# Performance work log

Measured on AMD Instinct MI355X. Metric: run time of the kernel, lower is better.

## Reference

```python
import jax, jax.numpy as jnp
import numpy as np

B, L, D, HW = 128, 512, 512, 512
NEG = -1e9


def _ff(x, weights):
    # feed-forward chain: relu(x @ W) per layer
    for w in weights:
        x = jax.nn.relu(jnp.matmul(x, w))
    return x


def _masked_softmax_flat(logits, mask):
    # softmax over the flattened last axis, masked entries excluded
    logits = jnp.where(mask > 0, logits, NEG)
    return jax.nn.softmax(logits, axis=-1)


def setup_inputs() -> dict:
    key = jax.random.key(0)
    ks = jax.random.split(key, 11)
    u = lambda k, shape: jax.random.uniform(k, shape, jnp.float32, -0.05, 0.05)
    return {
        "premise": jax.random.normal(ks[0], (B, L, D), jnp.float32),
        "hypothesis": jax.random.normal(ks[1], (B, L, D), jnp.float32),
        "premise_mask": jax.random.randint(ks[2], (B, L), 0, 2, jnp.int32),
        "hypothesis_mask": jax.random.randint(ks[3], (B, L), 0, 2, jnp.int32),
        "attend_w0": u(ks[4], (D, HW)),
        "attend_w1": u(ks[5], (HW, HW)),
        "compare_w0": u(ks[6], (2 * D, HW)),
        "compare_w1": u(ks[7], (HW, HW)),
        "aggregate_w0": u(ks[8], (2 * HW, HW)),
        "aggregate_w1": u(ks[9], (HW, HW)),
        "scorer": u(ks[10], (HW, 2)),
    }


def reference(premise, hypothesis, premise_mask, hypothesis_mask,
              attend_w0, attend_w1, compare_w0, compare_w1,
              aggregate_w0, aggregate_w1, scorer):
    pm = premise_mask.astype(premise.dtype)      # [B, P]
    hm = hypothesis_mask.astype(hypothesis.dtype)  # [B, H]
    p_emb = premise * pm[..., None]              # zero out masked words
    h_emb = hypothesis * hm[..., None]

    # Attend: project with shared F, score all pairs
    proj_p = _ff(p_emb, [attend_w0, attend_w1])  # [B, P, HW]
    proj_h = _ff(h_emb, [attend_w0, attend_w1])  # [B, H, HW]
    att = jnp.einsum('bpd,bhd->bph', proj_p, proj_h)  # [B, P, H]
    Bn, P, H = att.shape

    # Faithful to original: softmax over the *flattened* P*H axis with pairwise mask
    p2h_mask = (pm[:, :, None] * hm[:, None, :]).reshape(Bn, P * H)
    h2p_mask = (hm[:, :, None] * pm[:, None, :]).reshape(Bn, H * P)
    p2h = _masked_softmax_flat(att.reshape(Bn, P * H), p2h_mask).reshape(Bn, P, H)
    h2p = _masked_softmax_flat(jnp.swapaxes(att, 1, 2).reshape(Bn, H * P), h2p_mask).reshape(Bn, H, P)

    # Weighted sums (alignments)
    p2h_align = jnp.einsum('bph,bhd->bpd', p2h, h_emb)  # [B, P, D]
    h2p_align = jnp.einsum('bhp,bpd->bhd', h2p, p_emb)  # [B, H, D]

    # Compare with shared G
    compared_p = _ff(jnp.concatenate([p_emb, p2h_align], axis=-1), [compare_w0, compare_w1])
    compared_h = _ff(jnp.concatenate([h_emb, h2p_align], axis=-1), [compare_w0, compare_w1])

    # Aggregate with H, then score
    aggregated = jnp.concatenate([compared_p.sum(axis=1), compared_h.sum(axis=1)], axis=-1)  # [B, 2*HW]
    hidden = _ff(aggregated, [aggregate_w0, aggregate_w1])  # [B, HW]
    return jax.nn.softmax(jnp.matmul(hidden, scorer), axis=-1)  # [B, 2]
```

## Files before the change

### kernel.cpp

```cpp
#include <hip/hip_runtime.h>
#include <hip/hip_bf16.h>
#include <stdint.h>

typedef unsigned short u16;
typedef uint8_t u8;
typedef __bf16 bf16x8 __attribute__((ext_vector_type(8)));
typedef float f32x4 __attribute__((ext_vector_type(4)));

__device__ __forceinline__ u16 f2b(float f){
  uint32_t u = __float_as_uint(f);
  u = (u + 0x7fffu + ((u >> 16) & 1u)) >> 16;
  return (u16)u;
}
__device__ __forceinline__ float b2f(u16 u){
  return __uint_as_float(((uint32_t)u) << 16);
}
__device__ __forceinline__ uint32_t f2e4(float f){
  uint32_t u = __float_as_uint(f);
  uint32_t s = (u >> 24) & 0x80u;
  uint32_t a = u & 0x7fffffffu;
  if (a >= 0x43e00000u) return s | 0x7eu;
  if (a < 0x3c800000u){
    float v = __uint_as_float(a) * 512.0f + 12582912.0f;
    return s | (__float_as_uint(v) & 7u);
  }
  uint32_t t = a - (120u << 23);
  t += 0x7ffffu + ((t >> 20) & 1u);
  return s | (t >> 20);
}

typedef const void __attribute__((address_space(1))) gv_t;
typedef void __attribute__((address_space(3))) sv_t;

__device__ __forceinline__ void gload16(const void* g, void* l){
  __builtin_amdgcn_global_load_lds((gv_t*)g, (sv_t*)l, 16, 0, 0);
}

__global__ __launch_bounds__(256) void cnt_scan(const int* __restrict__ pm,
    const int* __restrict__ hm, int* __restrict__ pfx, int* __restrict__ cnts)
{
  int bs = blockIdx.x;
  const int* msk = (bs < 128) ? pm + bs*512 : hm + (bs-128)*512;
  __shared__ int sA[256], sB[256], fl[512];
  int t = threadIdx.x;
  int a = (msk[2*t] != 0), b = (msk[2*t+1] != 0);
  fl[2*t] = a; fl[2*t+1] = b;
  sA[t] = a + b;
  __syncthreads();
  int* cur = sA; int* nxt = sB;
  #pragma unroll
  for (int off = 1; off < 256; off <<= 1){
    int v = cur[t] + ((t >= off) ? cur[t-off] : 0);
    nxt[t] = v;
    __syncthreads();
    int* tmp = cur; cur = nxt; nxt = tmp;
  }
  int incl = cur[t];
  int excl = incl - fl[2*t] - fl[2*t+1];
  pfx[bs*512 + 2*t]     = excl;
  pfx[bs*512 + 2*t + 1] = excl + fl[2*t];
  if (t == 255) cnts[bs] = incl;
}

__global__ __launch_bounds__(256) void gscan_k(const int* __restrict__ cnts,
    int* __restrict__ gpfx, int* __restrict__ hloc)
{
  __shared__ int sA[256], sB[256];
  int t = threadIdx.x;
  int v0 = cnts[t];
  sA[t] = v0;
  __syncthreads();
  int* cur = sA; int* nxt = sB;
  #pragma unroll
  for (int off = 1; off < 256; off <<= 1){
    int v = cur[t] + ((t >= off) ? cur[t-off] : 0);
    nxt[t] = v;
    __syncthreads();
    int* tmp = cur; cur = nxt; nxt = tmp;
  }
  int incl = cur[t];
  gpfx[t] = incl - v0;
  if (t == 255) gpfx[256] = incl;
  __syncthreads();
  if (t >= 128) hloc[t - 128] = (incl - v0) - cur[127];
}

__global__ __launch_bounds__(256) void compact_copy(
    const float* __restrict__ prem, const float* __restrict__ hyp,
    const int* __restrict__ pm, const int* __restrict__ hm,
    const int* __restrict__ pfx, const int* __restrict__ gpfx,
    u8* __restrict__ embC8, int* __restrict__ rowMap)
{
  int blk = blockIdx.x;
  int bs = blk >> 2, qtr = blk & 3;
  const float* src = (bs < 128) ? prem + (long)bs*262144 : hyp + (long)(bs-128)*262144;
  const int*  msk = (bs < 128) ? pm + bs*512 : hm + (bs-128)*512;
  const int*  pf  = pfx + bs*512;
  long gbase = gpfx[bs];
  int t = threadIdx.x;
  for (int idx = t; idx < 128*32; idx += 256){
    int r = qtr*128 + (idx >> 5);
    if (msk[r] == 0) continue;
    int c = (idx & 31) * 16;
    int dr = pf[r];
    long g = gbase + dr;
    if ((idx & 31) == 0) rowMap[g] = bs*512 + dr;
    const float4* s4 = (const float4*)(src + (long)r*512 + c);
    float4 v0 = s4[0], v1 = s4[1], v2 = s4[2], v3 = s4[3];
    union { u8 o[16]; uint4 q; } u;
    u.o[0]=f2e4(v0.x); u.o[1]=f2e4(v0.y); u.o[2]=f2e4(v0.z); u.o[3]=f2e4(v0.w);
    u.o[4]=f2e4(v1.x); u.o[5]=f2e4(v1.y); u.o[6]=f2e4(v1.z); u.o[7]=f2e4(v1.w);
    u.o[8]=f2e4(v2.x); u.o[9]=f2e4(v2.y); u.o[10]=f2e4(v2.z); u.o[11]=f2e4(v2.w);
    u.o[12]=f2e4(v3.x); u.o[13]=f2e4(v3.y); u.o[14]=f2e4(v3.z); u.o[15]=f2e4(v3.w);
    *(uint4*)&embC8[g*512 + c] = u.q;
  }
}

__global__ void wtrans3_k(const float* __restrict__ W0, const float* __restrict__ W1,
                          const float* __restrict__ W2, u8* __restrict__ O0,
                          u8* __restrict__ O1, u8* __restrict__ O2){
  __shared__ float tile[32][33];
  const float* W = (blockIdx.z == 0) ? W0 : (blockIdx.z == 1 ? W1 : W2);
  u8* out        = (blockIdx.z == 0) ? O0 : (blockIdx.z == 1 ? O1 : O2);
  int c0 = blockIdx.x*32, r0 = blockIdx.y*32;
  int tx = threadIdx.x & 31, ty = threadIdx.x >> 5;
  #pragma unroll
  for (int i = 0; i < 4; ++i){
    int rr = ty + i*8;
    tile[rr][tx] = W[(long)(r0+rr)*512 + c0 + tx];
  }
  __syncthreads();
  #pragma unroll
  for (int i = 0; i < 4; ++i){
    int rr = ty + i*8;
    out[(long)(c0+rr)*512 + r0 + tx] = (u8)f2e4(tile[tx][rr]);
  }
}
__global__ void wtrans_k(const float* __restrict__ W, u8* __restrict__ out, int R, int C){
  __shared__ float tile[32][33];
  int c0 = blockIdx.x*32, r0 = blockIdx.y*32;
  int tx = threadIdx.x & 31, ty = threadIdx.x >> 5;
  #pragma unroll
  for (int i = 0; i < 4; ++i){
    int rr = ty + i*8;
    tile[rr][tx] = W[(long)(r0+rr)*C + c0 + tx];
  }
  __syncthreads();
  #pragma unroll
  for (int i = 0; i < 4; ++i){
    int rr = ty + i*8;
    out[(long)(c0+rr)*R + r0 + tx] = (u8)f2e4(tile[tx][rr]);
  }
}

__global__ __launch_bounds__(256) void btrans2(const u8* __restrict__ in,
    const int* __restrict__ gpfx, const int* __restrict__ cnts,
    u8* __restrict__ outP, u8* __restrict__ outH)
{
  __shared__ u8 tile[64][72];
  int z = blockIdx.z;
  long sbase = (long)gpfx[z] * 512;
  int cnt = cnts[z];
  int r0 = blockIdx.y*64;
  if (r0 >= ((cnt + 63) & ~63)) return;
  u8* dst = (z < 128) ? outP + (long)z*262144 : outH + (long)(z-128)*262144;
  int c0 = blockIdx.x*64;
  int t = threadIdx.x;
  int rr = t >> 3, cc = (t & 7)*8;
  #pragma unroll
  for (int pass = 0; pass < 2; ++pass){
    int r = rr + pass*32;
    uint2 v = {0, 0};
    if (r0 + r < cnt) v = *(const uint2*)&in[sbase + (long)(r0+r)*512 + c0+cc];
    const u8* vv = (const u8*)&v;
    #pragma unroll
    for (int j = 0; j < 8; ++j) tile[r][cc+j] = vv[j];
  }
  __syncthreads();
  #pragma unroll
  for (int pass = 0; pass < 2; ++pass){
    int r = rr + pass*32;
    union { u8 o[8]; uint2 q2; } u;
    #pragma unroll
    for (int j = 0; j < 8; ++j) u.o[j] = tile[cc+j][r];
    *(uint2*)&dst[(long)(c0+r)*512 + r0+cc] = u.q2;
  }
}

template<int MODE, bool F8OUT>
__global__ __launch_bounds__(256) void gemm_nt(
    const u16* __restrict__ A0, const u16* __restrict__ Bt, void* __restrict__ Cout,
    const int* __restrict__ cnts, int cntMOff, int cntKOff,
    const int* __restrict__ goffA, const int* __restrict__ goffB, const int* __restrict__ goffC,
    float2* __restrict__ part,
    int N, int K, long sAb, long sBb, long sCb,
    int gyMask, int gyShift, int cpx)
{
  __shared__ u16 As[2][128*32];
  __shared__ u16 Bs[2][128*32];
  __shared__ float2 wred4[4];

  const int p = blockIdx.x;
  const int l = (p & 7)*cpx + (p >> 3);
  const int bx = l & 3;
  const int rest = l >> 2;
  const int by = rest & gyMask;
  const int bz = rest >> gyShift;
  const int ml = (by & 3) * 128;
  const int m0 = by*128, n0 = bx*128;
  const int t = threadIdx.x, lane = t & 63, wv = t >> 6;
  const int wm = wv >> 1, wn = wv & 1, r = lane & 15, q = lane >> 4;

  bool dead = (ml >= cnts[cntMOff + bz]);
  if (MODE == 3 && !dead) dead = (n0 >= cnts[128 + bz]);
  if (dead){
    if (MODE == 3 && t == 0) part[bz*16 + by*4 + bx] = float2{-3.0e38f, 0.f};
    return;
  }

  int Keff = K;
  if (cntKOff >= 0){
    int kc = cnts[cntKOff + bz];
    Keff = (kc + 31) & ~31;
    if (Keff < 32) Keff = 32;
  }
  const int nt = Keff >> 5;

  const u16* a0 = A0 + (goffA ? 0 : (long)bz*sAb);
  const long aro = (goffA ? goffA[bz] : 0);
  const u16* bt = Bt + (goffB ? 0 : (long)bz*sBb);
  const long bro = (goffB ? goffB[bz] : 0);

  f32x4 acc[4][4] = {};

  auto stage = [&](int buf, int k0){
    #pragma unroll
    for (int h = 0; h < 2; ++h){
      int c = t + h*256;
      int row = c >> 2;
      int qg = (c & 3) ^ ((row >> 1) & 3);
      int ks = k0 + qg*8;
      gload16(a0 + (aro + m0 + row)*512 + ks, &As[buf][c*8]);
      gload16(bt + (bro + n0 + row)*(long)K + ks, &Bs[buf][c*8]);
    }
  };

  stage(0, 0);
  __syncthreads();
  for (int it = 0; it < nt; ++it){
    const int cur = it & 1;
    if (it + 1 < nt) stage(cur ^ 1, (it + 1) << 5);
    bf16x8 af[4], bfr[4];
    #pragma unroll
    for (int mi = 0; mi < 4; ++mi){
      int row = wm*64 + mi*16 + r;
      af[mi] = *reinterpret_cast<const bf16x8*>(&As[cur][(row*4 + (q ^ ((row>>1)&3)))*8]);
    }
    #pragma unroll
    for (int ni = 0; ni < 4; ++ni){
      int row = wn*64 + ni*16 + r;
      bfr[ni] = *reinterpret_cast<const bf16x8*>(&Bs[cur][(row*4 + (q ^ ((row>>1)&3)))*8]);
    }
    #pragma unroll
    for (int mi = 0; mi < 4; ++mi)
      #pragma unroll
      for (int ni = 0; ni < 4; ++ni)
        acc[mi][ni] = __builtin_amdgcn_mfma_f32_16x16x32_bf16(af[mi], bfr[ni], acc[mi][ni], 0, 0, 0);
    __syncthreads();
  }

  if constexpr (MODE == 3){
    const int cp = cnts[bz], ch = cnts[128 + bz];
    int hc[4];
    #pragma unroll
    for (int ni = 0; ni < 4; ++ni) hc[ni] = (n0 + wn*64 + ni*16 + r) < ch;
    float tm = -3.0e38f, ts = 0.f;
    #pragma unroll
    for (int mi = 0; mi < 4; ++mi){
      #pragma unroll
      for (int i = 0; i < 4; ++i){
        int rr = m0 + wm*64 + mi*16 + q*4 + i;
        int prm = rr < cp;
        #pragma unroll
        for (int ni = 0; ni < 4; ++ni){
          float v = acc[mi][ni][i];
          int cc = n0 + wn*64 + ni*16 + r;
          ((u16*)Cout)[(long)bz*sCb + (long)rr*N + cc] = f2b(v);
          float lv = (prm && hc[ni]) ? v : -1.0e9f;
          float nm = fmaxf(tm, lv);
          ts = ts*__expf(tm - nm) + __expf(lv - nm);
          tm = nm;
        }
      }
    }
    #pragma unroll
    for (int d = 1; d < 64; d <<= 1){
      float om = __shfl_xor(tm, d), os = __shfl_xor(ts, d);
      float nm = fmaxf(tm, om);
      ts = ts*__expf(tm - nm) + os*__expf(om - nm);
      tm = nm;
    }
    if (lane == 0) wred4[wv] = float2{tm, ts};
    __syncthreads();
    if (t == 0){
      float m = wred4[0].x, s = wred4[0].y;
      #pragma unroll
      for (int w = 1; w < 4; ++w){
        float om = wred4[w].x, os = wred4[w].y, nm = fmaxf(m, om);
        s = s*__expf(m - nm) + os*__expf(om - nm); m = nm;
      }
      part[bz*16 + by*4 + bx] = float2{m, s};
    }
  } else {
    const long co = goffC[bz];
    const int lim = cnts[cntMOff + bz];
    #pragma unroll
    for (int mi = 0; mi < 4; ++mi){
      #pragma unroll
      for (int ni = 0; ni < 4; ++ni){
        int cc = n0 + wn*64 + ni*16 + r;
        #pragma unroll
        for (int i = 0; i < 4; ++i){
          int rr = m0 + wm*64 + mi*16 + q*4 + i;
          if (rr < lim){
            if (F8OUT) ((u8*)Cout)[(co + rr)*512 + cc] = (u8)f2e4(acc[mi][ni][i]);
            else       ((u16*)Cout)[(co + rr)*(long)N + cc] = f2b(acc[mi][ni][i]);
          }
        }
      }
    }
  }
}

template<int MODE, int OUTT, bool SPLIT>
__global__ __launch_bounds__(256) void gemm_p8(
    const u8* __restrict__ A0, const u8* __restrict__ AP1, const u8* __restrict__ AH1,
    const u8* __restrict__ Bt, void* __restrict__ Cout, float* __restrict__ aggOut,
    const int* __restrict__ gpfx, const int* __restrict__ rowMap, int K, int cpx)
{
  __shared__ __align__(16) u8 As[2][128*64];
  __shared__ __align__(16) u8 Bs[2][128*64];
  __shared__ float redbuf[3][128];

  int Mtot = gpfx[256]; if (Mtot > 81920) Mtot = 81920;
  const int Mp = SPLIT ? gpfx[128] : 0;
  const int p = blockIdx.x;
  const int l = (p & 7)*cpx + (p >> 3);
  const int bx = l & 3, by = l >> 2;
  const int m0 = by*128, n0 = bx*128;
  if (m0 >= Mtot) return;
  const int t = threadIdx.x, lane = t & 63, wv = t >> 6;
  const int wm = wv >> 1, wn = wv & 1, r = lane & 15, q = lane >> 4;

  f32x4 acc[4][4] = {};
  const int nt = K >> 6;

  auto stage = [&](int buf, int kb){
    #pragma unroll
    for (int h = 0; h < 2; ++h){
      int c = t + h*256;
      int row = c >> 2, pp = c & 3;
      int ks = kb + ((pp ^ ((row >> 1) & 3)) << 4);
      int gr = m0 + row;
      const u8* sA;
      if (SPLIT && ks >= 512)
        sA = (gr < Mp ? AP1 + (long)gr*512 : AH1 + (long)(gr - Mp)*512) + (ks - 512);
      else
        sA = A0 + (long)gr*512 + ks;
      gload16(sA, &As[buf][c*16]);
      gload16(Bt + (long)(n0 + row)*K + ks, &Bs[buf][c*16]);
    }
  };

  stage(0, 0);
  __syncthreads();
  for (int it = 0; it < nt; ++it){
    const int cur = it & 1;
    if (it + 1 < nt) stage(cur ^ 1, (it + 1) << 6);
    long afL[2][4], bfL[2][4];
    #pragma unroll
    for (int s = 0; s < 2; ++s){
      const int j = s*4 + q;
      #pragma unroll
      for (int mi = 0; mi < 4; ++mi){
        int row = wm*64 + mi*16 + r;
        afL[s][mi] = *(const long*)&As[cur][row*64 + ((((j>>1) ^ ((row>>1)&3))<<4) | ((j&1)<<3))];
      }
      #pragma unroll
      for (int ni = 0; ni < 4; ++ni){
        int row = wn*64 + ni*16 + r;
        bfL[s][ni] = *(const long*)&Bs[cur][row*64 + ((((j>>1) ^ ((row>>1)&3))<<4) | ((j&1)<<3))];
      }
    }
    #pragma unroll
    for (int s = 0; s < 2; ++s)
      #pragma unroll
      for (int mi = 0; mi < 4; ++mi)
        #pragma unroll
        for (int ni = 0; ni < 4; ++ni)
          acc[mi][ni] = __builtin_amdgcn_mfma_f32_16x16x32_fp8_fp8(afL[s][mi], bfL[s][ni], acc[mi][ni], 0, 0, 0);
    __syncthreads();
  }

  if constexpr (MODE == 0){
    #pragma unroll
    for (int mi = 0; mi < 4; ++mi){
      #pragma unroll
      for (int i = 0; i < 4; ++i){
        int gr = m0 + wm*64 + mi*16 + q*4 + i;
        if (gr >= Mtot) continue;
        #pragma unroll
        for (int ni = 0; ni < 4; ++ni){
          int cc = n0 + wn*64 + ni*16 + r;
          float v = fmaxf(acc[mi][ni][i], 0.f);
          if (OUTT == 0) ((u8*)Cout)[(long)gr*512 + cc] = (u8)f2e4(v);
          else           ((u16*)Cout)[(long)gr*512 + cc] = f2b(v);
        }
      }
    }
  } else {
    for (int i = t; i < 3*128; i += 256) ((float*)redbuf)[i] = 0.f;
    __syncthreads();
    const int side0 = rowMap[m0] >> 9;
    int slr[4][4];
    #pragma unroll
    for (int mi = 0; mi < 4; ++mi)
      #pragma unroll
      for (int i = 0; i < 4; ++i){
        int gr = m0 + wm*64 + mi*16 + q*4 + i;
        slr[mi][i] = (gr < Mtot) ? ((rowMap[gr] >> 9) - side0) : -1;
      }
    #pragma unroll
    for (int ni = 0; ni < 4; ++ni){
      float va = 0.f, vb = 0.f, vc = 0.f;
      #pragma unroll
      for (int mi = 0; mi < 4; ++mi)
        #pragma unroll
        for (int i = 0; i < 4; ++i){
          int sl = slr[mi][i];
          if (sl < 0) continue;
          float rv = fmaxf(acc[mi][ni][i], 0.f);
          if (sl == 0) va += rv; else if (sl == 1) vb += rv; else vc += rv;
        }
      int cc = wn*64 + ni*16 + r;
      if (va != 0.f) atomicAdd(&redbuf[0][cc], va);
      if (vb != 0.f) atomicAdd(&redbuf[1][cc], vb);
      if (vc != 0.f) atomicAdd(&redbuf[2][cc], vc);
    }
    __syncthreads();
    if (t < 128){
      #pragma unroll
      for (int sl = 0; sl < 3; ++sl){
        int side = side0 + sl;
        float v = redbuf[sl][t];
        if (side < 256 && v != 0.f) atomicAdd(&aggOut[(long)side*512 + t + n0], v);
      }
    }
  }
}

__global__ __launch_bounds__(256) void gemm_a8(
    const u8* __restrict__ P2H, const u8* __restrict__ H2P,
    const u8* __restrict__ PT8, const u8* __restrict__ HT8,
    u8* __restrict__ AP, u8* __restrict__ AH,
    const int* __restrict__ cnts, const int* __restrict__ gpfx, const int* __restrict__ hloc)
{
  __shared__ __align__(16) u8 As[2][128*64];
  __shared__ __align__(16) u8 Bs[2][128*64];
  const int p = blockIdx.x;
  const int l = (p & 7)*512 + (p >> 3);
  const int side = l >> 11;
  const int r2 = l & 2047;
  const int bx = r2 & 3, by = (r2 >> 2) & 3, bz = r2 >> 4;
  const int Mlive = side ? cnts[128 + bz] : cnts[bz];
  const int m0 = by*128, n0 = bx*128;
  if (m0 >= Mlive) return;
  const int Klive = side ? cnts[bz] : cnts[128 + bz];
  int Keff = (Klive + 63) & ~63; if (Keff < 64) Keff = 64;
  const int nt = Keff >> 6;
  const long abase = side ? (long)hloc[bz] : (long)gpfx[bz];
  const u8* A0 = (side ? H2P : P2H) + abase*512;
  const u8* Bt = (side ? PT8 : HT8) + (long)bz*262144;
  u8* Cp = (side ? AH : AP) + abase*512;
  const int t = threadIdx.x, lane = t & 63, wv = t >> 6;
  const int wm = wv >> 1, wn = wv & 1, r = lane & 15, q = lane >> 4;

  f32x4 acc[4][4] = {};

  auto stage = [&](int buf, int kb){
    #pragma unroll
    for (int h = 0; h < 2; ++h){
      int c = t + h*256;
      int row = c >> 2, pp = c & 3;
      int ks = kb + ((pp ^ ((row >> 1) & 3)) << 4);
      gload16(A0 + (long)(m0 + row)*512 + ks, &As[buf][c*16]);
      gload16(Bt + (long)(n0 + row)*512 + ks, &Bs[buf][c*16]);
    }
  };

  stage(0, 0);
  __syncthreads();
  for (int it = 0; it < nt; ++it){
    const int cur = it & 1;
    if (it + 1 < nt) stage(cur ^ 1, (it + 1) << 6);
    long afL[2][4], bfL[2][4];
    #pragma unroll
    for (int s = 0; s < 2; ++s){
      const int j = s*4 + q;
      #pragma unroll
      for (int mi = 0; mi < 4; ++mi){
        int row = wm*64 + mi*16 + r;
        afL[s][mi] = *(const long*)&As[cur][row*64 + ((((j>>1) ^ ((row>>1)&3))<<4) | ((j&1)<<3))];
      }
      #pragma unroll
      for (int ni = 0; ni < 4; ++ni){
        int row = wn*64 + ni*16 + r;
        bfL[s][ni] = *(const long*)&Bs[cur][row*64 + ((((j>>1) ^ ((row>>1)&3))<<4) | ((j&1)<<3))];
      }
    }
    #pragma unroll
    for (int s = 0; s < 2; ++s)
      #pragma unroll
      for (int mi = 0; mi < 4; ++mi)
        #pragma unroll
        for (int ni = 0; ni < 4; ++ni)
          acc[mi][ni] = __builtin_amdgcn_mfma_f32_16x16x32_fp8_fp8(afL[s][mi], bfL[s][ni], acc[mi][ni], 0, 0, 0);
    __syncthreads();
  }

  #pragma unroll
  for (int mi = 0; mi < 4; ++mi){
    #pragma unroll
    for (int i = 0; i < 4; ++i){
      int lr = m0 + wm*64 + mi*16 + q*4 + i;
      if (lr >= Mlive) continue;
      #pragma unroll
      for (int ni = 0; ni < 4; ++ni){
        int cc = n0 + wn*64 + ni*16 + r;
        Cp[(long)lr*512 + cc] = (u8)f2e4(acc[mi][ni][i]);
      }
    }
  }
}

__global__ void sm_merge(const float2* __restrict__ part, float2* __restrict__ bms){
  int b = threadIdx.x;
  float m = -3.0e38f, s = 0.f;
  for (int i = 0; i < 16; ++i){
    float2 p = part[b*16 + i];
    float nm = fmaxf(m, p.x);
    s = s*__expf(m - nm) + p.y*__expf(p.x - nm);
    m = nm;
  }
  bms[b] = float2{m, 1.0f / s};
}

__global__ __launch_bounds__(256) void sm_write_t(const u16* __restrict__ att,
    const int* __restrict__ cnts, const int* __restrict__ gpfx, const int* __restrict__ hloc,
    const float2* __restrict__ bms, u8* __restrict__ p2h, u8* __restrict__ h2p)
{
  __shared__ u8 tile[64][72];
  int b = blockIdx.z, h0 = blockIdx.x*64, p0 = blockIdx.y*64;
  int cp = cnts[b], ch = cnts[128 + b];
  int cp64 = (cp + 63) & ~63, ch64 = (ch + 63) & ~63;
  bool needP = (p0 < cp) && (h0 < ch64);
  bool needH = (h0 < ch) && (p0 < cp64);
  if (!needP && !needH) return;
  float2 ms = bms[b];
  int t = threadIdx.x;
  int rr = t >> 3, cc = (t & 7)*8;
  long base = (long)b*262144;
  long pbase = gpfx[b];
  long hbase = hloc[b];
  #pragma unroll
  for (int pass = 0; pass < 2; ++pass){
    int pr = rr + pass*32;
    uint4 v = *(const uint4*)&att[base + (long)(p0+pr)*512 + h0+cc];
    const u16* vv = (const u16*)&v;
    int pa = (p0 + pr) < cp;
    union { u8 o[8]; uint2 q2; } u;
    #pragma unroll
    for (int j = 0; j < 8; ++j){
      float x = b2f(vv[j]);
      u.o[j] = (pa && (h0+cc+j) < ch) ? (u8)f2e4(__expf(x - ms.x)*ms.y) : (u8)0;
    }
    if (pa) *(uint2*)&p2h[(pbase + p0+pr)*512 + h0+cc] = u.q2;
    #pragma unroll
    for (int j = 0; j < 8; ++j) tile[pr][cc+j] = u.o[j];
  }
  __syncthreads();
  #pragma unroll
  for (int pass = 0; pass < 2; ++pass){
    int hr = rr + pass*32;
    if (h0 + hr < ch){
      union { u8 o[8]; uint2 q2; } u;
      #pragma unroll
      for (int j = 0; j < 8; ++j) u.o[j] = tile[cc+j][hr];
      *(uint2*)&h2p[(hbase + h0+hr)*512 + p0+cc] = u.q2;
    }
  }
}

__global__ __launch_bounds__(256) void ff1_k(const float* __restrict__ agg,
    const float* __restrict__ g0, float* __restrict__ tt)
{
  __shared__ float xs[256];
  int b = blockIdx.y, kc = blockIdx.x, t = threadIdx.x;
  int kbase = kc*256;
  {
    int kk = kbase + t;
    xs[t] = (kk < 512) ? agg[b*512 + kk] : agg[(long)(128 + b)*512 + (kk - 512)];
  }
  __syncthreads();
  float ax = 0.f, ay = 0.f;
  #pragma unroll 4
  for (int k = 0; k < 256; ++k){
    float2 g = *(const float2*)(g0 + (long)(kbase + k)*512 + 2*t);
    ax += xs[k]*g.x; ay += xs[k]*g.y;
  }
  atomicAdd(&tt[b*512 + 2*t],     ax);
  atomicAdd(&tt[b*512 + 2*t + 1], ay);
}

__global__ __launch_bounds__(256) void ff2_k(const float* __restrict__ tt,
    const float* __restrict__ g1, float* __restrict__ x2)
{
  __shared__ float xs[128];
  int b = blockIdx.y, kc = blockIdx.x, t = threadIdx.x;
  int kbase = kc*128;
  if (t < 128) xs[t] = fmaxf(tt[b*512 + kbase + t], 0.f);
  __syncthreads();
  float ax = 0.f, ay = 0.f;
  #pragma unroll 4
  for (int k = 0; k < 128; ++k){
    float2 g = *(const float2*)(g1 + (long)(kbase + k)*512 + 2*t);
    ax += xs[k]*g.x; ay += xs[k]*g.y;
  }
  atomicAdd(&x2[b*512 + 2*t],     ax);
  atomicAdd(&x2[b*512 + 2*t + 1], ay);
}

__global__ __launch_bounds__(64) void score_k(const float* __restrict__ x2,
    const float* __restrict__ sc, float* __restrict__ out)
{
  int b = blockIdx.x, t = threadIdx.x;
  float s0 = 0.f, s1 = 0.f;
  for (int k = t; k < 512; k += 64){
    float v = fmaxf(x2[b*512 + k], 0.f);
    s0 += v*sc[2*k]; s1 += v*sc[2*k + 1];
  }
  #pragma unroll
  for (int d = 1; d < 64; d <<= 1){ s0 += __shfl_xor(s0, d); s1 += __shfl_xor(s1, d); }
  if (t == 0){
    float mm = fmaxf(s0, s1);
    float e0 = __expf(s0 - mm), e1 = __expf(s1 - mm);
    float inv = 1.f / (e0 + e1);
    out[2*b]     = e0*inv;
    out[2*b + 1] = e1*inv;
  }
}

extern "C" void kernel_launch(void* const* d_in, const int* in_sizes, int n_in,
                              void* d_out, int out_size, void* d_ws, size_t ws_size,
                              hipStream_t stream) {
  const float* premise    = (const float*)d_in[0];
  const float* hypothesis = (const float*)d_in[1];
  const int*   pm         = (const int*)d_in[2];
  const int*   hm         = (const int*)d_in[3];
  const float* w_a0       = (const float*)d_in[4];
  const float* w_a1       = (const float*)d_in[5];
  const float* w_c0       = (const float*)d_in[6];
  const float* w_c1       = (const float*)d_in[7];
  const float* w_g0       = (const float*)d_in[8];
  const float* w_g1       = (const float*)d_in[9];
  const float* w_sc       = (const float*)d_in[10];
  float* out = (float*)d_out;

  const size_t MB = 1ull << 20;
  if (ws_size < 456*MB) return;

  char* ws = (char*)d_ws;
  u8*  embC8 = (u8*)(ws + 0);
  u8*  t08   = (u8*)(ws + 40*MB);
  u8*  ap8   = (u8*)(ws + 40*MB);
  u8*  ah8   = (u8*)(ws + 60*MB);
  u16* proj  = (u16*)(ws + 80*MB);
  u8*  cmp8  = (u8*)(ws + 80*MB);
  u8*  pT8   = (u8*)(ws + 160*MB);
  u8*  hT8   = (u8*)(ws + 200*MB);
  u16* att_b = (u16*)(ws + 288*MB);
  u8*  p2h8  = (u8*)(ws + 352*MB);
  u8*  h2p8  = (u8*)(ws + 372*MB);
  u8*  wt_a0 = (u8*)(ws + 432*MB);
  u8*  wt_a1 = (u8*)(ws + 432*MB + 256*1024);
  u8*  wt_c1 = (u8*)(ws + 432*MB + 512*1024);
  u8*  wt_c0 = (u8*)(ws + 433*MB);
  float* agg = (float*)(ws + 434*MB);
  float* tt  = (float*)(ws + 434*MB + 512*1024);
  float* x2  = (float*)(ws + 434*MB + 768*1024);
  int*   pfx = (int*)(ws + 435*MB);
  int* rowMap= (int*)(ws + 436*MB);
  int*  gpfx = (int*)(ws + 437*MB);
  int*  hloc = (int*)(ws + 437*MB + 4096);
  int*  cnts = (int*)(ws + 437*MB + 8192);
  float2* part = (float2*)(ws + 437*MB + 12288);
  float2* bms  = (float2*)(ws + 437*MB + 32768);

  const long S = 262144;

  cnt_scan<<<256, 256, 0, stream>>>(pm, hm, pfx, cnts);
  gscan_k<<<1, 256, 0, stream>>>(cnts, gpfx, hloc);
  compact_copy<<<1024, 256, 0, stream>>>(premise, hypothesis, pm, hm, pfx, gpfx, embC8, rowMap);

  wtrans3_k<<<dim3(16,16,3), 256, 0, stream>>>(w_a0, w_a1, w_c1, wt_a0, wt_a1, wt_c1);
  wtrans_k<<<dim3(16,32), 256, 0, stream>>>(w_c0, wt_c0, 1024, 512);
  hipMemsetAsync(agg, 0, 256*512*sizeof(float), stream);
  hipMemsetAsync(tt,  0, 128*512*sizeof(float), stream);
  hipMemsetAsync(x2,  0, 128*512*sizeof(float), stream);

  gemm_p8<0,0,false><<<2112, 256, 0, stream>>>(embC8, nullptr, nullptr, wt_a0, t08, nullptr, gpfx, nullptr, 512, 264);
  gemm_p8<0,1,false><<<2112, 256, 0, stream>>>(t08, nullptr, nullptr, wt_a1, proj, nullptr, gpfx, nullptr, 512, 264);

  btrans2<<<dim3(8,8,256), 256, 0, stream>>>(embC8, gpfx, cnts, pT8, hT8);

  gemm_nt<3,false><<<2048, 256, 0, stream>>>(proj, proj, att_b, cnts, 0, -1,
      gpfx, gpfx + 128, nullptr, part, 512, 512, 0, 0, S, 3, 2, 256);

  sm_merge<<<1, 128, 0, stream>>>(part, bms);
  sm_write_t<<<dim3(8,8,128), 256, 0, stream>>>(att_b, cnts, gpfx, hloc, bms, p2h8, h2p8);

  gemm_a8<<<4096, 256, 0, stream>>>(p2h8, h2p8, pT8, hT8, ap8, ah8, cnts, gpfx, hloc);

  gemm_p8<0,0,true><<<2112, 256, 0, stream>>>(embC8, ap8, ah8, wt_c0, cmp8, nullptr, gpfx, nullptr, 1024, 264);

  gemm_p8<2,0,false><<<2112, 256, 0, stream>>>(cmp8, nullptr, nullptr, wt_c1, nullptr, agg, gpfx, rowMap, 512, 264);

  ff1_k<<<dim3(4,128), 256, 0, stream>>>(agg, w_g0, tt);
  ff2_k<<<dim3(4,128), 256, 0, stream>>>(tt, w_g1, x2);
  score_k<<<128, 64, 0, stream>>>(x2, w_sc, out);
}
```

Before: 453.6 us.

## Shrink GEMM N-tile to 64 and move attention score GEMM to FP8

All fp8 GEMM kernels now use 128x64 tiles instead of 128x128, which doubles the block count and is meant to improve occupancy and load balance across CUs. The attention projection output is now stored as FP8 rather than bf16, and a new fp8 MFMA kernel (gemm_t8) replaces the bf16 gemm_nt for the attention scores. It keeps the fused per-tile online-softmax partials, now with 32 partials per batch. This halves the projection traffic and uses faster fp8 MFMA, at the cost of lower precision in the attention logits and more A-tile reloads per output.

```diff
diff --git a/kernel.cpp b/kernel.cpp
--- a/kernel.cpp
+++ b/kernel.cpp
@@ -187,172 +187,27 @@
   }
 }
 
-template<int MODE, bool F8OUT>
-__global__ __launch_bounds__(256) void gemm_nt(
-    const u16* __restrict__ A0, const u16* __restrict__ Bt, void* __restrict__ Cout,
-    const int* __restrict__ cnts, int cntMOff, int cntKOff,
-    const int* __restrict__ goffA, const int* __restrict__ goffB, const int* __restrict__ goffC,
-    float2* __restrict__ part,
-    int N, int K, long sAb, long sBb, long sCb,
-    int gyMask, int gyShift, int cpx)
-{
-  __shared__ u16 As[2][128*32];
-  __shared__ u16 Bs[2][128*32];
-  __shared__ float2 wred4[4];
-
-  const int p = blockIdx.x;
-  const int l = (p & 7)*cpx + (p >> 3);
-  const int bx = l & 3;
-  const int rest = l >> 2;
-  const int by = rest & gyMask;
-  const int bz = rest >> gyShift;
-  const int ml = (by & 3) * 128;
-  const int m0 = by*128, n0 = bx*128;
-  const int t = threadIdx.x, lane = t & 63, wv = t >> 6;
-  const int wm = wv >> 1, wn = wv & 1, r = lane & 15, q = lane >> 4;
-
-  bool dead = (ml >= cnts[cntMOff + bz]);
-  if (MODE == 3 && !dead) dead = (n0 >= cnts[128 + bz]);
-  if (dead){
-    if (MODE == 3 && t == 0) part[bz*16 + by*4 + bx] = float2{-3.0e38f, 0.f};
-    return;
-  }
-
-  int Keff = K;
-  if (cntKOff >= 0){
-    int kc = cnts[cntKOff + bz];
-    Keff = (kc + 31) & ~31;
-    if (Keff < 32) Keff = 32;
-  }
-  const int nt = Keff >> 5;
-
-  const u16* a0 = A0 + (goffA ? 0 : (long)bz*sAb);
-  const long aro = (goffA ? goffA[bz] : 0);
-  const u16* bt = Bt + (goffB ? 0 : (long)bz*sBb);
-  const long bro = (goffB ? goffB[bz] : 0);
-
-  f32x4 acc[4][4] = {};
-
-  auto stage = [&](int buf, int k0){
-    #pragma unroll
-    for (int h = 0; h < 2; ++h){
-      int c = t + h*256;
-      int row = c >> 2;
-      int qg = (c & 3) ^ ((row >> 1) & 3);
-      int ks = k0 + qg*8;
-      gload16(a0 + (aro + m0 + row)*512 + ks, &As[buf][c*8]);
-      gload16(bt + (bro + n0 + row)*(long)K + ks, &Bs[buf][c*8]);
-    }
-  };
-
-  stage(0, 0);
-  __syncthreads();
-  for (int it = 0; it < nt; ++it){
-    const int cur = it & 1;
-    if (it + 1 < nt) stage(cur ^ 1, (it + 1) << 5);
-    bf16x8 af[4], bfr[4];
-    #pragma unroll
-    for (int mi = 0; mi < 4; ++mi){
-      int row = wm*64 + mi*16 + r;
-      af[mi] = *reinterpret_cast<const bf16x8*>(&As[cur][(row*4 + (q ^ ((row>>1)&3)))*8]);
-    }
-    #pragma unroll
-    for (int ni = 0; ni < 4; ++ni){
-      int row = wn*64 + ni*16 + r;
-      bfr[ni] = *reinterpret_cast<const bf16x8*>(&Bs[cur][(row*4 + (q ^ ((row>>1)&3)))*8]);
-    }
-    #pragma unroll
-    for (int mi = 0; mi < 4; ++mi)
-      #pragma unroll
-      for (int ni = 0; ni < 4; ++ni)
-        acc[mi][ni] = __builtin_amdgcn_mfma_f32_16x16x32_bf16(af[mi], bfr[ni], acc[mi][ni], 0, 0, 0);
-    __syncthreads();
-  }
-
-  if constexpr (MODE == 3){
-    const int cp = cnts[bz], ch = cnts[128 + bz];
-    int hc[4];
-    #pragma unroll
-    for (int ni = 0; ni < 4; ++ni) hc[ni] = (n0 + wn*64 + ni*16 + r) < ch;
-    float tm = -3.0e38f, ts = 0.f;
-    #pragma unroll
-    for (int mi = 0; mi < 4; ++mi){
-      #pragma unroll
-      for (int i = 0; i < 4; ++i){
-        int rr = m0 + wm*64 + mi*16 + q*4 + i;
-        int prm = rr < cp;
-        #pragma unroll
-        for (int ni = 0; ni < 4; ++ni){
-          float v = acc[mi][ni][i];
-          int cc = n0 + wn*64 + ni*16 + r;
-          ((u16*)Cout)[(long)bz*sCb + (long)rr*N + cc] = f2b(v);
-          float lv = (prm && hc[ni]) ? v : -1.0e9f;
-          float nm = fmaxf(tm, lv);
-          ts = ts*__expf(tm - nm) + __expf(lv - nm);
-          tm = nm;
-        }
-      }
-    }
-    #pragma unroll
-    for (int d = 1; d < 64; d <<= 1){
-      float om = __shfl_xor(tm, d), os = __shfl_xor(ts, d);
-      float nm = fmaxf(tm, om);
-      ts = ts*__expf(tm - nm) + os*__expf(om - nm);
-      tm = nm;
-    }
-    if (lane == 0) wred4[wv] = float2{tm, ts};
-    __syncthreads();
-    if (t == 0){
-      float m = wred4[0].x, s = wred4[0].y;
-      #pragma unroll
-      for (int w = 1; w < 4; ++w){
-        float om = wred4[w].x, os = wred4[w].y, nm = fmaxf(m, om);
-        s = s*__expf(m - nm) + os*__expf(om - nm); m = nm;
-      }
-      part[bz*16 + by*4 + bx] = float2{m, s};
-    }
-  } else {
-    const long co = goffC[bz];
-    const int lim = cnts[cntMOff + bz];
-    #pragma unroll
-    for (int mi = 0; mi < 4; ++mi){
-      #pragma unroll
-      for (int ni = 0; ni < 4; ++ni){
-        int cc = n0 + wn*64 + ni*16 + r;
-        #pragma unroll
-        for (int i = 0; i < 4; ++i){
-          int rr = m0 + wm*64 + mi*16 + q*4 + i;
-          if (rr < lim){
-            if (F8OUT) ((u8*)Cout)[(co + rr)*512 + cc] = (u8)f2e4(acc[mi][ni][i]);
-            else       ((u16*)Cout)[(co + rr)*(long)N + cc] = f2b(acc[mi][ni][i]);
-          }
-        }
-      }
-    }
-  }
-}
-
-template<int MODE, int OUTT, bool SPLIT>
+template<int MODE, bool SPLIT>
 __global__ __launch_bounds__(256) void gemm_p8(
     const u8* __restrict__ A0, const u8* __restrict__ AP1, const u8* __restrict__ AH1,
     const u8* __restrict__ Bt, void* __restrict__ Cout, float* __restrict__ aggOut,
     const int* __restrict__ gpfx, const int* __restrict__ rowMap, int K, int cpx)
 {
   __shared__ __align__(16) u8 As[2][128*64];
-  __shared__ __align__(16) u8 Bs[2][128*64];
-  __shared__ float redbuf[3][128];
+  __shared__ __align__(16) u8 Bs[2][64*64];
+  __shared__ float redbuf[3][64];
 
   int Mtot = gpfx[256]; if (Mtot > 81920) Mtot = 81920;
   const int Mp = SPLIT ? gpfx[128] : 0;
   const int p = blockIdx.x;
   const int l = (p & 7)*cpx + (p >> 3);
-  const int bx = l & 3, by = l >> 2;
-  const int m0 = by*128, n0 = bx*128;
+  const int bx = l & 7, by = l >> 3;
+  const int m0 = by*128, n0 = bx*64;
   if (m0 >= Mtot) return;
   const int t = threadIdx.x, lane = t & 63, wv = t >> 6;
   const int wm = wv >> 1, wn = wv & 1, r = lane & 15, q = lane >> 4;
 
-  f32x4 acc[4][4] = {};
+  f32x4 acc[4][2] = {};
   const int nt = K >> 6;
 
   auto stage = [&](int buf, int kb){
@@ -368,6 +223,11 @@
       else
         sA = A0 + (long)gr*512 + ks;
       gload16(sA, &As[buf][c*16]);
+    }
+    {
+      int c = t;
+      int row = c >> 2, pp = c & 3;
+      int ks = kb + ((pp ^ ((row >> 1) & 3)) << 4);
       gload16(Bt + (long)(n0 + row)*K + ks, &Bs[buf][c*16]);
     }
   };
@@ -377,7 +237,7 @@
   for (int it = 0; it < nt; ++it){
     const int cur = it & 1;
     if (it + 1 < nt) stage(cur ^ 1, (it + 1) << 6);
-    long afL[2][4], bfL[2][4];
+    long afL[2][4], bfL[2][2];
     #pragma unroll
     for (int s = 0; s < 2; ++s){
       const int j = s*4 + q;
@@ -387,8 +247,8 @@
         afL[s][mi] = *(const long*)&As[cur][row*64 + ((((j>>1) ^ ((row>>1)&3))<<4) | ((j&1)<<3))];
       }
       #pragma unroll
-      for (int ni = 0; ni < 4; ++ni){
-        int row = wn*64 + ni*16 + r;
+      for (int ni = 0; ni < 2; ++ni){
+        int row = wn*32 + ni*16 + r;
         bfL[s][ni] = *(const long*)&Bs[cur][row*64 + ((((j>>1) ^ ((row>>1)&3))<<4) | ((j&1)<<3))];
       }
     }
@@ -397,7 +257,7 @@
       #pragma unroll
       for (int mi = 0; mi < 4; ++mi)
         #pragma unroll
-        for (int ni = 0; ni < 4; ++ni)
+        for (int ni = 0; ni < 2; ++ni)
           acc[mi][ni] = __builtin_amdgcn_mfma_f32_16x16x32_fp8_fp8(afL[s][mi], bfL[s][ni], acc[mi][ni], 0, 0, 0);
     __syncthreads();
   }
@@ -410,16 +270,14 @@
         int gr = m0 + wm*64 + mi*16 + q*4 + i;
         if (gr >= Mtot) continue;
         #pragma unroll
-        for (int ni = 0; ni < 4; ++ni){
-          int cc = n0 + wn*64 + ni*16 + r;
-          float v = fmaxf(acc[mi][ni][i], 0.f);
-          if (OUTT == 0) ((u8*)Cout)[(long)gr*512 + cc] = (u8)f2e4(v);
-          else           ((u16*)Cout)[(long)gr*512 + cc] = f2b(v);
+        for (int ni = 0; ni < 2; ++ni){
+          int cc = n0 + wn*32 + ni*16 + r;
+          ((u8*)Cout)[(long)gr*512 + cc] = (u8)f2e4(fmaxf(acc[mi][ni][i], 0.f));
         }
       }
     }
   } else {
-    for (int i = t; i < 3*128; i += 256) ((float*)redbuf)[i] = 0.f;
+    for (int i = t; i < 3*64; i += 256) ((float*)redbuf)[i] = 0.f;
     __syncthreads();
     const int side0 = rowMap[m0] >> 9;
     int slr[4][4];
@@ -431,7 +289,7 @@
         slr[mi][i] = (gr < Mtot) ? ((rowMap[gr] >> 9) - side0) : -1;
       }
     #pragma unroll
-    for (int ni = 0; ni < 4; ++ni){
+    for (int ni = 0; ni < 2; ++ni){
       float va = 0.f, vb = 0.f, vc = 0.f;
       #pragma unroll
       for (int mi = 0; mi < 4; ++mi)
@@ -442,18 +300,18 @@
           float rv = fmaxf(acc[mi][ni][i], 0.f);
           if (sl == 0) va += rv; else if (sl == 1) vb += rv; else vc += rv;
         }
-      int cc = wn*64 + ni*16 + r;
+      int cc = wn*32 + ni*16 + r;
       if (va != 0.f) atomicAdd(&redbuf[0][cc], va);
       if (vb != 0.f) atomicAdd(&redbuf[1][cc], vb);
       if (vc != 0.f) atomicAdd(&redbuf[2][cc], vc);
     }
     __syncthreads();
-    if (t < 128){
+    if (t < 64){
       #pragma unroll
       for (int sl = 0; sl < 3; ++sl){
         int side = side0 + sl;
         float v = redbuf[sl][t];
-        if (side < 256 && v != 0.f) atomicAdd(&aggOut[(long)side*512 + t + n0], v);
+        if (side < 256 && v != 0.f) atomicAdd(&aggOut[(long)side*512 + n0 + t], v);
       }
     }
   }
@@ -466,14 +324,14 @@
     const int* __restrict__ cnts, const int* __restrict__ gpfx, const int* __restrict__ hloc)
 {
   __shared__ __align__(16) u8 As[2][128*64];
-  __shared__ __align__(16) u8 Bs[2][128*64];
+  __shared__ __align__(16) u8 Bs[2][64*64];
   const int p = blockIdx.x;
-  const int l = (p & 7)*512 + (p >> 3);
-  const int side = l >> 11;
-  const int r2 = l & 2047;
-  const int bx = r2 & 3, by = (r2 >> 2) & 3, bz = r2 >> 4;
+  const int l = (p & 7)*1024 + (p >> 3);
+  const int side = l >> 12;
+  const int r2 = l & 4095;
+  const int bx = r2 & 7, by = (r2 >> 3) & 3, bz = r2 >> 5;
   const int Mlive = side ? cnts[128 + bz] : cnts[bz];
-  const int m0 = by*128, n0 = bx*128;
+  const int m0 = by*128, n0 = bx*64;
   if (m0 >= Mlive) return;
   const int Klive = side ? cnts[bz] : cnts[128 + bz];
   int Keff = (Klive + 63) & ~63; if (Keff < 64) Keff = 64;
@@ -485,7 +343,7 @@
   const int t = threadIdx.x, lane = t & 63, wv = t >> 6;
   const int wm = wv >> 1, wn = wv & 1, r = lane & 15, q = lane >> 4;
 
-  f32x4 acc[4][4] = {};
+  f32x4 acc[4][2] = {};
 
   auto stage = [&](int buf, int kb){
     #pragma unroll
@@ -494,6 +352,11 @@
       int row = c >> 2, pp = c & 3;
       int ks = kb + ((pp ^ ((row >> 1) & 3)) << 4);
       gload16(A0 + (long)(m0 + row)*512 + ks, &As[buf][c*16]);
+    }
+    {
+      int c = t;
+      int row = c >> 2, pp = c & 3;
+      int ks = kb + ((pp ^ ((row >> 1) & 3)) << 4);
       gload16(Bt + (long)(n0 + row)*512 + ks, &Bs[buf][c*16]);
     }
   };
@@ -503,7 +366,7 @@
   for (int it = 0; it < nt; ++it){
     const int cur = it & 1;
     if (it + 1 < nt) stage(cur ^ 1, (it + 1) << 6);
-    long afL[2][4], bfL[2][4];
+    long afL[2][4], bfL[2][2];
     #pragma unroll
     for (int s = 0; s < 2; ++s){
       const int j = s*4 + q;
@@ -513,8 +376,8 @@
         afL[s][mi] = *(const long*)&As[cur][row*64 + ((((j>>1) ^ ((row>>1)&3))<<4) | ((j&1)<<3))];
       }
       #pragma unroll
-      for (int ni = 0; ni < 4; ++ni){
-        int row = wn*64 + ni*16 + r;
+      for (int ni = 0; ni < 2; ++ni){
+        int row = wn*32 + ni*16 + r;
         bfL[s][ni] = *(const long*)&Bs[cur][row*64 + ((((j>>1) ^ ((row>>1)&3))<<4) | ((j&1)<<3))];
       }
     }
@@ -523,7 +386,7 @@
       #pragma unroll
       for (int mi = 0; mi < 4; ++mi)
         #pragma unroll
-        for (int ni = 0; ni < 4; ++ni)
+        for (int ni = 0; ni < 2; ++ni)
           acc[mi][ni] = __builtin_amdgcn_mfma_f32_16x16x32_fp8_fp8(afL[s][mi], bfL[s][ni], acc[mi][ni], 0, 0, 0);
     __syncthreads();
   }
@@ -535,19 +398,131 @@
       int lr = m0 + wm*64 + mi*16 + q*4 + i;
       if (lr >= Mlive) continue;
       #pragma unroll
-      for (int ni = 0; ni < 4; ++ni){
-        int cc = n0 + wn*64 + ni*16 + r;
+      for (int ni = 0; ni < 2; ++ni){
+        int cc = n0 + wn*32 + ni*16 + r;
         Cp[(long)lr*512 + cc] = (u8)f2e4(acc[mi][ni][i]);
       }
     }
+  }
+}
+
+__global__ __launch_bounds__(256) void gemm_t8(
+    const u8* __restrict__ proj8, u16* __restrict__ attOut,
+    const int* __restrict__ cnts, const int* __restrict__ gpfx,
+    float2* __restrict__ part)
+{
+  __shared__ __align__(16) u8 As[2][128*64];
+  __shared__ __align__(16) u8 Bs[2][64*64];
+  __shared__ float2 wred4[4];
+  const int p = blockIdx.x;
+  const int l = (p & 7)*512 + (p >> 3);
+  const int bx = l & 7, by = (l >> 3) & 3, bz = l >> 5;
+  const int cp = cnts[bz], ch = cnts[128 + bz];
+  const int m0 = by*128, n0 = bx*64;
+  const int t = threadIdx.x, lane = t & 63, wv = t >> 6;
+  if (m0 >= cp || n0 >= ch){
+    if (t == 0) part[bz*32 + by*8 + bx] = float2{-3.0e38f, 0.f};
+    return;
+  }
+  const u8* A0 = proj8 + (long)gpfx[bz]*512;
+  const u8* Bt = proj8 + (long)gpfx[128 + bz]*512;
+  const int wm = wv >> 1, wn = wv & 1, r = lane & 15, q = lane >> 4;
+
+  f32x4 acc[4][2] = {};
+
+  auto stage = [&](int buf, int kb){
+    #pragma unroll
+    for (int h = 0; h < 2; ++h){
+      int c = t + h*256;
+      int row = c >> 2, pp = c & 3;
+      int ks = kb + ((pp ^ ((row >> 1) & 3)) << 4);
+      gload16(A0 + (long)(m0 + row)*512 + ks, &As[buf][c*16]);
+    }
+    {
+      int c = t;
+      int row = c >> 2, pp = c & 3;
+      int ks = kb + ((pp ^ ((row >> 1) & 3)) << 4);
+      gload16(Bt + (long)(n0 + row)*512 + ks, &Bs[buf][c*16]);
+    }
+  };
+
+  stage(0, 0);
+  __syncthreads();
+  for (int it = 0; it < 8; ++it){
+    const int cur = it & 1;
+    if (it + 1 < 8) stage(cur ^ 1, (it + 1) << 6);
+    long afL[2][4], bfL[2][2];
+    #pragma unroll
+    for (int s = 0; s < 2; ++s){
+      const int j = s*4 + q;
+      #pragma unroll
+      for (int mi = 0; mi < 4; ++mi){
+        int row = wm*64 + mi*16 + r;
+        afL[s][mi] = *(const long*)&As[cur][row*64 + ((((j>>1) ^ ((row>>1)&3))<<4) | ((j&1)<<3))];
+      }
+      #pragma unroll
+      for (int ni = 0; ni < 2; ++ni){
+        int row = wn*32 + ni*16 + r;
+        bfL[s][ni] = *(const long*)&Bs[cur][row*64 + ((((j>>1) ^ ((row>>1)&3))<<4) | ((j&1)<<3))];
+      }
+    }
+    #pragma unroll
+    for (int s = 0; s < 2; ++s)
+      #pragma unroll
+      for (int mi = 0; mi < 4; ++mi)
+        #pragma unroll
+        for (int ni = 0; ni < 2; ++ni)
+          acc[mi][ni] = __builtin_amdgcn_mfma_f32_16x16x32_fp8_fp8(afL[s][mi], bfL[s][ni], acc[mi][ni], 0, 0, 0);
+    __syncthreads();
+  }
+
+  int hc[2];
+  #pragma unroll
+  for (int ni = 0; ni < 2; ++ni) hc[ni] = (n0 + wn*32 + ni*16 + r) < ch;
+  float tm = -3.0e38f, ts = 0.f;
+  #pragma unroll
+  for (int mi = 0; mi < 4; ++mi){
+    #pragma unroll
+    for (int i = 0; i < 4; ++i){
+      int rr = m0 + wm*64 + mi*16 + q*4 + i;
+      int prm = rr < cp;
+      #pragma unroll
+      for (int ni = 0; ni < 2; ++ni){
+        float v = acc[mi][ni][i];
+        int cc = n0 + wn*32 + ni*16 + r;
+        attOut[(long)bz*262144 + (long)rr*512 + cc] = f2b(v);
+        float lv = (prm && hc[ni]) ? v : -1.0e9f;
+        float nm = fmaxf(tm, lv);
+        ts = ts*__expf(tm - nm) + __expf(lv - nm);
+        tm = nm;
+      }
+    }
+  }
+  #pragma unroll
+  for (int d = 1; d < 64; d <<= 1){
+    float om = __shfl_xor(tm, d), os = __shfl_xor(ts, d);
+    float nm = fmaxf(tm, om);
+    ts = ts*__expf(tm - nm) + os*__expf(om - nm);
+    tm = nm;
+  }
+  if (lane == 0) wred4[wv] = float2{tm, ts};
+  __syncthreads();
+  if (t == 0){
+    float m = wred4[0].x, s = wred4[0].y;
+    #pragma unroll
+    for (int w = 1; w < 4; ++w){
+      float om = wred4[w].x, os = wred4[w].y, nm = fmaxf(m, om);
+      s = s*__expf(m - nm) + os*__expf(om - nm); m = nm;
+    }
+    part[bz*32 + by*8 + bx] = float2{m, s};
   }
 }
 
 __global__ void sm_merge(const float2* __restrict__ part, float2* __restrict__ bms){
   int b = threadIdx.x;
   float m = -3.0e38f, s = 0.f;
-  for (int i = 0; i < 16; ++i){
-    float2 p = part[b*16 + i];
+  for (int i = 0; i < 32; ++i){
+    float2 p = part[b*32 + i];
     float nm = fmaxf(m, p.x);
     s = s*__expf(m - nm) + p.y*__expf(p.x - nm);
     m = nm;
@@ -684,7 +659,7 @@
   u8*  t08   = (u8*)(ws + 40*MB);
   u8*  ap8   = (u8*)(ws + 40*MB);
   u8*  ah8   = (u8*)(ws + 60*MB);
-  u16* proj  = (u16*)(ws + 80*MB);
+  u8*  proj8 = (u8*)(ws + 80*MB);
   u8*  cmp8  = (u8*)(ws + 80*MB);
   u8*  pT8   = (u8*)(ws + 160*MB);
   u8*  hT8   = (u8*)(ws + 200*MB);
@@ -704,9 +679,7 @@
   int*  hloc = (int*)(ws + 437*MB + 4096);
   int*  cnts = (int*)(ws + 437*MB + 8192);
   float2* part = (float2*)(ws + 437*MB + 12288);
-  float2* bms  = (float2*)(ws + 437*MB + 32768);
-
-  const long S = 262144;
+  float2* bms  = (float2*)(ws + 437*MB + 49152);
 
   cnt_scan<<<256, 256, 0, stream>>>(pm, hm, pfx, cnts);
   gscan_k<<<1, 256, 0, stream>>>(cnts, gpfx, hloc);
@@ -718,22 +691,21 @@
   hipMemsetAsync(tt,  0, 128*512*sizeof(float), stream);
   hipMemsetAsync(x2,  0, 128*512*sizeof(float), stream);
 
-  gemm_p8<0,0,false><<<2112, 256, 0, stream>>>(embC8, nullptr, nullptr, wt_a0, t08, nullptr, gpfx, nullptr, 512, 264);
-  gemm_p8<0,1,false><<<2112, 256, 0, stream>>>(t08, nullptr, nullptr, wt_a1, proj, nullptr, gpfx, nullptr, 512, 264);
+  gemm_p8<0,false><<<5120, 256, 0, stream>>>(embC8, nullptr, nullptr, wt_a0, t08, nullptr, gpfx, nullptr, 512, 640);
+  gemm_p8<0,false><<<5120, 256, 0, stream>>>(t08, nullptr, nullptr, wt_a1, proj8, nullptr, gpfx, nullptr, 512, 640);
 
   btrans2<<<dim3(8,8,256), 256, 0, stream>>>(embC8, gpfx, cnts, pT8, hT8);
 
-  gemm_nt<3,false><<<2048, 256, 0, stream>>>(proj, proj, att_b, cnts, 0, -1,
-      gpfx, gpfx + 128, nullptr, part, 512, 512, 0, 0, S, 3, 2, 256);
+  gemm_t8<<<4096, 256, 0, stream>>>(proj8, att_b, cnts, gpfx, part);
 
   sm_merge<<<1, 128, 0, stream>>>(part, bms);
   sm_write_t<<<dim3(8,8,128), 256, 0, stream>>>(att_b, cnts, gpfx, hloc, bms, p2h8, h2p8);
 
-  gemm_a8<<<4096, 256, 0, stream>>>(p2h8, h2p8, pT8, hT8, ap8, ah8, cnts, gpfx, hloc);
-
-  gemm_p8<0,0,true><<<2112, 256, 0, stream>>>(embC8, ap8, ah8, wt_c0, cmp8, nullptr, gpfx, nullptr, 1024, 264);
-
-  gemm_p8<2,0,false><<<2112, 256, 0, stream>>>(cmp8, nullptr, nullptr, wt_c1, nullptr, agg, gpfx, rowMap, 512, 264);
+  gemm_a8<<<8192, 256, 0, stream>>>(p2h8, h2p8, pT8, hT8, ap8, ah8, cnts, gpfx, hloc);
+
+  gemm_p8<0,true><<<5120, 256, 0, stream>>>(embC8, ap8, ah8, wt_c0, cmp8, nullptr, gpfx, nullptr, 1024, 640);
+
+  gemm_p8<2,false><<<5120, 256, 0, stream>>>(cmp8, nullptr, nullptr, wt_c1, nullptr, agg, gpfx, rowMap, 512, 640);
 
   ff1_k<<<dim3(4,128), 256, 0, stream>>>(agg, w_g0, tt);
   ff2_k<<<dim3(4,128), 256, 0, stream>>>(tt, w_g1, x2);
```

After: 457.9 us. No clear change (+0.9%).
